# Performance work log

Hardware: AMD Instinct MI355X
Metric: run time of the kernel (lower is better)

Reference implementation:

```python
import jax, jax.numpy as jnp
import numpy as np

N_NODES = 100000
N_EDGES = 3200000
D_IN, D_HID, D_OUT = 512, 16, 64


def setup_inputs() -> dict:
    key = jax.random.key(0)
    ks = jax.random.split(key, 7)
    x = jax.random.normal(ks[0], (N_NODES, D_IN), jnp.float32)
    edge_index = jax.random.randint(ks[1], (2, N_EDGES), 0, N_NODES, dtype=jnp.int32)
    edge_weight = jax.random.uniform(ks[2], (N_EDGES,), jnp.float32)
    W1 = jax.random.normal(ks[3], (D_IN, D_HID), jnp.float32) * (1.0 / np.sqrt(D_IN))
    b1 = jnp.zeros((D_HID,), jnp.float32)
    W2 = jax.random.normal(ks[4], (D_HID, D_OUT), jnp.float32) * (1.0 / np.sqrt(D_HID))
    b2 = jnp.zeros((D_OUT,), jnp.float32)
    return {"x": x, "edge_index": edge_index, "edge_weight": edge_weight,
            "W1": W1, "b1": b1, "W2": W2, "b2": b2}


def reference(x, edge_index, edge_weight, W1, b1, W2, b2):
    N = x.shape[0]
    loop = jnp.arange(N, dtype=edge_index.dtype)
    # GCNConv(normalize=True): add self-loops (weight 1), symmetric normalization
    src = jnp.concatenate([edge_index[0], loop])
    dst = jnp.concatenate([edge_index[1], loop])
    w = jnp.concatenate([edge_weight, jnp.ones((N,), x.dtype)])
    deg = jax.ops.segment_sum(w, dst, num_segments=N)
    dinv = jnp.where(deg > 0, jax.lax.rsqrt(deg), 0.0)
    norm = dinv[src] * w * dinv[dst]  # [E+N]

    def gcn_conv(h, W, b):
        h = h @ W  # transform first (thin GEMM), then aggregate
        msg = h[src] * norm[:, None]  # gather + scale
        return jax.ops.segment_sum(msg, dst, num_segments=N) + b  # scatter-add

    h = jax.nn.relu(gcn_conv(x, W1, b1))
    # F.dropout is identity in eval mode
    out = gcn_conv(h, W2, b2)
    return jax.nn.log_softmax(out, axis=1)
```

## Files before the change

### kernel.cpp

```cpp
#include <hip/hip_runtime.h>
#include <hip/hip_bf16.h>


#define D_IN 512
#define D_HID 16
#define D_OUT 64
#define BDIM 128
#define BSHIFT 7
#define NBLK0 512

__global__ __launch_bounds__(256) void p0_count(const int* __restrict__ dst,
                                                int* __restrict__ bcnt,
                                                int NBUCK, int E, int chunk) {
    extern __shared__ int hist[];
    int k = blockIdx.x;
    for (int i = threadIdx.x; i < NBUCK; i += 256) hist[i] = 0;
    __syncthreads();
    int beg = k * chunk, end = min(beg + chunk, E);
    for (int e = beg + threadIdx.x; e < end; e += 256)
        atomicAdd(&hist[dst[e] >> BSHIFT], 1);
    __syncthreads();
    for (int i = threadIdx.x; i < NBUCK; i += 256)
        bcnt[(size_t)k * NBUCK + i] = hist[i];
}

__global__ __launch_bounds__(256) void p_scan1(int* __restrict__ bcnt,
                                               int* __restrict__ btot, int NBUCK) {
    __shared__ int s[256];
    int b = blockIdx.x, t = threadIdx.x;
    int v0 = bcnt[(size_t)(2 * t) * NBUCK + b];
    int v1 = bcnt[(size_t)(2 * t + 1) * NBUCK + b];
    int pair = v0 + v1;
    s[t] = pair;
    __syncthreads();
    for (int off = 1; off < 256; off <<= 1) {
        int v = (t >= off) ? s[t - off] : 0;
        __syncthreads();
        s[t] += v;
        __syncthreads();
    }
    int ex = s[t] - pair;
    bcnt[(size_t)(2 * t) * NBUCK + b] = ex;
    bcnt[(size_t)(2 * t + 1) * NBUCK + b] = ex + v0;
    if (t == 255) btot[b] = s[255];
}

__global__ __launch_bounds__(1024) void p_scan2(const int* __restrict__ btot,
                                                int* __restrict__ bbase,
                                                int NBUCK, int E) {
    __shared__ int s[1024];
    int t = threadIdx.x;
    int v = (t < NBUCK) ? btot[t] : 0;
    s[t] = v;
    __syncthreads();
    for (int off = 1; off < 1024; off <<= 1) {
        int u = (t >= off) ? s[t - off] : 0;
        __syncthreads();
        s[t] += u;
        __syncthreads();
    }
    if (t < NBUCK) bbase[t] = s[t] - v;
    if (t == 0) bbase[NBUCK] = E;
}

__global__ __launch_bounds__(256) void p1_scatter(const int* __restrict__ src,
                                                  const int* __restrict__ dst,
                                                  const float* __restrict__ w,
                                                  const int* __restrict__ bcnt,
                                                  const int* __restrict__ bbase,
                                                  float2* __restrict__ tmp,
                                                  int NBUCK, int E, int chunk) {
    extern __shared__ int cur[];
    int k = blockIdx.x;
    for (int i = threadIdx.x; i < NBUCK; i += 256)
        cur[i] = bbase[i] + bcnt[(size_t)k * NBUCK + i];
    __syncthreads();
    int beg = k * chunk, end = min(beg + chunk, E);
    for (int e = beg + threadIdx.x; e < end; e += 256) {
        int d = dst[e];
        int b = d >> BSHIFT;
        int pos = atomicAdd(&cur[b], 1);
        tmp[pos] = make_float2(__int_as_float(((d & (BDIM - 1)) << 24) | src[e]), w[e]);
    }
}

__global__ __launch_bounds__(256) void p4_sort(const float2* __restrict__ tmp,
                                               const int* __restrict__ bbase,
                                               float2* __restrict__ sorted,
                                               int* __restrict__ row_start,
                                               float* __restrict__ dinv,
                                               int NBUCK, int N, int E) {
    __shared__ int cnt[BDIM];
    __shared__ float wdeg[BDIM];
    __shared__ int pre[BDIM];
    __shared__ int cur[BDIM];
    int b = blockIdx.x;
    if (threadIdx.x < BDIM) { cnt[threadIdx.x] = 0; wdeg[threadIdx.x] = 0.0f; }
    __syncthreads();
    int beg = bbase[b], end = bbase[b + 1];
    for (int e = beg + threadIdx.x; e < end; e += 256) {
        float2 p = tmp[e];
        int dl = ((unsigned)__float_as_int(p.x)) >> 24;
        atomicAdd(&cnt[dl], 1);
        atomicAdd(&wdeg[dl], p.y);
    }
    __syncthreads();
    if (threadIdx.x < BDIM) pre[threadIdx.x] = cnt[threadIdx.x];
    __syncthreads();
    for (int off = 1; off < BDIM; off <<= 1) {
        int add = 0;
        if (threadIdx.x < BDIM && threadIdx.x >= off) add = pre[threadIdx.x - off];
        __syncthreads();
        if (threadIdx.x < BDIM) pre[threadIdx.x] += add;
        __syncthreads();
    }
    if (threadIdx.x < BDIM) {
        int ex = beg + pre[threadIdx.x] - cnt[threadIdx.x];
        cur[threadIdx.x] = ex;
        int node = (b << BSHIFT) + threadIdx.x;
        if (node < N) {
            row_start[node] = ex;
            dinv[node] = __frsqrt_rn(1.0f + wdeg[threadIdx.x]);
        }
    }
    if (b == NBUCK - 1 && threadIdx.x == 0) row_start[N] = E;
    __syncthreads();
    for (int e = beg + threadIdx.x; e < end; e += 256) {
        float2 p = tmp[e];
        unsigned u = (unsigned)__float_as_int(p.x);
        int dl = u >> 24;
        int pos = atomicAdd(&cur[dl], 1);
        sorted[pos] = make_float2(__int_as_float((int)(u & 0xFFFFFFu)), p.y);
    }
}

__global__ __launch_bounds__(256) void gemm1_kernel(const float* __restrict__ x,
                                                    const float* __restrict__ W1,
                                                    float* __restrict__ t, int N) {
    __shared__ float w1t[16 * 520];
    for (int idx = threadIdx.x; idx < D_IN * D_HID; idx += 256) {
        int k = idx >> 4, j = idx & 15;
        w1t[j * 520 + k] = W1[idx];
    }
    __syncthreads();

    const int wave = threadIdx.x >> 6;
    const int lane = threadIdx.x & 63;
    const int g = lane >> 4;
    const int s = lane & 15;

    for (int base = blockIdx.x * 16; base < N; base += gridDim.x * 16) {
        int row = base + wave * 4 + g;
        if (row < N) {
            const float4* xr = (const float4*)(x + (size_t)row * D_IN);
            float4 xv[8];
#pragma unroll
            for (int i = 0; i < 8; ++i) xv[i] = xr[s + 16 * i];
            float acc[16];
#pragma unroll
            for (int j = 0; j < 16; ++j) acc[j] = 0.0f;
#pragma unroll
            for (int i = 0; i < 8; ++i) {
                int kb = 4 * s + 64 * i;
#pragma unroll
                for (int j = 0; j < 16; ++j) {
                    const float4 wv = *(const float4*)&w1t[j * 520 + kb];
                    acc[j] += xv[i].x * wv.x + xv[i].y * wv.y + xv[i].z * wv.z + xv[i].w * wv.w;
                }
            }
#pragma unroll
            for (int j = 0; j < 16; ++j) {
#pragma unroll
                for (int m = 1; m < 16; m <<= 1) acc[j] += __shfl_xor(acc[j], m, 64);
            }
            float v = acc[0];
#pragma unroll
            for (int j = 1; j < 16; ++j) v = (s == j) ? acc[j] : v;
            t[(size_t)row * 16 + s] = v;
        }
    }
}

template <int LAYER>
__global__ __launch_bounds__(256) void agg_kernel(const float2* __restrict__ sorted,
                                                  const int* __restrict__ row_start,
                                                  const float* __restrict__ feat,
                                                  const float* __restrict__ selfv,
                                                  const float* __restrict__ dinv,
                                                  const float* __restrict__ b1,
                                                  float* __restrict__ outp, int N) {
    int node = blockIdx.x * 4 + (threadIdx.x >> 6);
    if (node >= N) return;
    int lane = threadIdx.x & 63;
    int j = lane & 15, k = lane >> 4;
    int beg = row_start[node], end = row_start[node + 1];
    float acc = 0.0f;
    for (int e = beg + k; e < end; e += 4) {
        float2 p = sorted[e];
        int s = __float_as_int(p.x);
        acc += dinv[s] * p.y * feat[(size_t)s * 16 + j];
    }
    acc += __shfl_xor(acc, 16, 64);
    acc += __shfl_xor(acc, 32, 64);
    float dn = dinv[node];
    float sv = selfv[(size_t)node * 16 + j];
    float r = dn * acc + dn * dn * sv;
    if (LAYER == 1) r = fmaxf(r + b1[j], 0.0f);
    if (k == 0) outp[(size_t)node * 16 + j] = r;
}

__global__ __launch_bounds__(256) void out_kernel(const float* __restrict__ v,
                                                  const float* __restrict__ W2,
                                                  const float* __restrict__ b2,
                                                  float* __restrict__ out, int N) {
    __shared__ float w2s[16 * 64];
    __shared__ float b2s[64];
    for (int idx = threadIdx.x; idx < 16 * 64; idx += 256) w2s[idx] = W2[idx];
    if (threadIdx.x < 64) b2s[threadIdx.x] = b2[threadIdx.x];
    __syncthreads();

    const int wave = threadIdx.x >> 6;
    const int lane = threadIdx.x & 63;

    for (int node = blockIdx.x * 4 + wave; node < N; node += gridDim.x * 4) {
        const float4* v4 = (const float4*)(v + (size_t)node * 16);
        float z = b2s[lane];
#pragma unroll
        for (int q = 0; q < 4; ++q) {
            float4 a = v4[q];
            z += a.x * w2s[(4 * q + 0) * 64 + lane];
            z += a.y * w2s[(4 * q + 1) * 64 + lane];
            z += a.z * w2s[(4 * q + 2) * 64 + lane];
            z += a.w * w2s[(4 * q + 3) * 64 + lane];
        }
        float m = z;
#pragma unroll
        for (int off = 32; off; off >>= 1) m = fmaxf(m, __shfl_xor(m, off, 64));
        float ez = __expf(z - m);
        float ssum = ez;
#pragma unroll
        for (int off = 32; off; off >>= 1) ssum += __shfl_xor(ssum, off, 64);
        out[(size_t)node * 64 + lane] = z - m - __logf(ssum);
    }
}

extern "C" void kernel_launch(void* const* d_in, const int* in_sizes, int n_in,
                              void* d_out, int out_size, void* d_ws, size_t ws_size,
                              hipStream_t stream) {
    const float* x  = (const float*)d_in[0];
    const int*   ei = (const int*)d_in[1];
    const float* ew = (const float*)d_in[2];
    const float* W1 = (const float*)d_in[3];
    const float* b1 = (const float*)d_in[4];
    const float* W2 = (const float*)d_in[5];
    const float* b2 = (const float*)d_in[6];
    float* out = (float*)d_out;

    const int N = in_sizes[0] / D_IN;
    const int E = in_sizes[2];
    const int* srcI = ei;
    const int* dstI = ei + E;

    const int NBUCK = (N + BDIM - 1) >> BSHIFT;
    const int chunk = (E + NBLK0 - 1) / NBLK0;

    float* ws = (float*)d_ws;
    size_t o = 0;
    float* dinv      = ws + o;         o += (size_t)N;             o = (o + 3) & ~(size_t)3;
    int*   row_start = (int*)(ws + o); o += (size_t)N + 2;         o = (o + 3) & ~(size_t)3;
    int*   bbase     = (int*)(ws + o); o += (size_t)NBUCK + 1;     o = (o + 3) & ~(size_t)3;
    int*   btot      = (int*)(ws + o); o += (size_t)NBUCK;         o = (o + 3) & ~(size_t)3;
    int*   bcnt      = (int*)(ws + o); o += (size_t)NBLK0 * NBUCK; o = (o + 3) & ~(size_t)3;
    float* tmpR      = ws + o;
    size_t tmpsz = (size_t)2 * E; if ((size_t)32 * N > tmpsz) tmpsz = (size_t)32 * N;
    o += tmpsz;                                                    o = (o + 3) & ~(size_t)3;

    float2* tmp = (float2*)tmpR;
    float*  t   = tmpR;
    float*  h1  = tmpR + (size_t)16 * N;
    float*  v   = t;

    float2* sorted = ((size_t)out_size >= (size_t)E * 8)
                         ? (float2*)d_out
                         : (float2*)(ws + o);

    p0_count<<<NBLK0, 256, NBUCK * sizeof(int), stream>>>(dstI, bcnt, NBUCK, E, chunk);
    p_scan1<<<NBUCK, 256, 0, stream>>>(bcnt, btot, NBUCK);
    p_scan2<<<1, 1024, 0, stream>>>(btot, bbase, NBUCK, E);
    p1_scatter<<<NBLK0, 256, NBUCK * sizeof(int), stream>>>(srcI, dstI, ew, bcnt, bbase,
                                                            tmp, NBUCK, E, chunk);
    p4_sort<<<NBUCK, 256, 0, stream>>>(tmp, bbase, sorted, row_start, dinv, NBUCK, N, E);

    gemm1_kernel<<<1024, 256, 0, stream>>>(x, W1, t, N);

    agg_kernel<1><<<(N + 3) / 4, 256, 0, stream>>>(sorted, row_start, t, t, dinv, b1, h1, N);
    agg_kernel<2><<<(N + 3) / 4, 256, 0, stream>>>(sorted, row_start, h1, h1, dinv, b1, v, N);

    out_kernel<<<2048, 256, 0, stream>>>(v, W2, b2, out, N);
}
```

Before: 657.9 us.

## Precompute edge norms in CSR, vectorize aggregation, fuse output GEMM+softmax into layer-2

Splits the per-bucket sort into a count kernel and a scatter kernel. The scatter now stores the fully normalized edge weight, so the aggregation kernels no longer gather dinv[src] for every edge on every layer. Aggregation reads two edges per float4 load, with peeling for odd start and end indices. The second aggregation also fuses the W2 projection, bias and log_softmax, which removes the separate out_kernel and the round trip of the intermediate features. The cost is one extra kernel launch and a dinv gather inside the scatter, and the sorted edge buffer now always lives in the workspace.

```diff
diff --git a/kernel.cpp b/kernel.cpp
--- a/kernel.cpp
+++ b/kernel.cpp
@@ -84,16 +84,14 @@
     }
 }
 
-__global__ __launch_bounds__(256) void p4_sort(const float2* __restrict__ tmp,
-                                               const int* __restrict__ bbase,
-                                               float2* __restrict__ sorted,
-                                               int* __restrict__ row_start,
-                                               float* __restrict__ dinv,
-                                               int NBUCK, int N, int E) {
+__global__ __launch_bounds__(256) void p4a_count(const float2* __restrict__ tmp,
+                                                 const int* __restrict__ bbase,
+                                                 int* __restrict__ row_start,
+                                                 float* __restrict__ dinv,
+                                                 int NBUCK, int N, int E) {
     __shared__ int cnt[BDIM];
     __shared__ float wdeg[BDIM];
     __shared__ int pre[BDIM];
-    __shared__ int cur[BDIM];
     int b = blockIdx.x;
     if (threadIdx.x < BDIM) { cnt[threadIdx.x] = 0; wdeg[threadIdx.x] = 0.0f; }
     __syncthreads();
@@ -115,22 +113,38 @@
         __syncthreads();
     }
     if (threadIdx.x < BDIM) {
-        int ex = beg + pre[threadIdx.x] - cnt[threadIdx.x];
-        cur[threadIdx.x] = ex;
         int node = (b << BSHIFT) + threadIdx.x;
         if (node < N) {
-            row_start[node] = ex;
+            row_start[node] = beg + pre[threadIdx.x] - cnt[threadIdx.x];
             dinv[node] = __frsqrt_rn(1.0f + wdeg[threadIdx.x]);
         }
     }
     if (b == NBUCK - 1 && threadIdx.x == 0) row_start[N] = E;
-    __syncthreads();
+}
+
+__global__ __launch_bounds__(256) void p4b_scatter(const float2* __restrict__ tmp,
+                                                   const int* __restrict__ bbase,
+                                                   const int* __restrict__ row_start,
+                                                   const float* __restrict__ dinv,
+                                                   float2* __restrict__ sorted, int N) {
+    __shared__ int cur[BDIM];
+    __shared__ float dl_dinv[BDIM];
+    int b = blockIdx.x;
+    if (threadIdx.x < BDIM) {
+        int node = (b << BSHIFT) + threadIdx.x;
+        cur[threadIdx.x] = (node < N) ? row_start[node] : 0;
+        dl_dinv[threadIdx.x] = (node < N) ? dinv[node] : 0.0f;
+    }
+    __syncthreads();
+    int beg = bbase[b], end = bbase[b + 1];
     for (int e = beg + threadIdx.x; e < end; e += 256) {
         float2 p = tmp[e];
         unsigned u = (unsigned)__float_as_int(p.x);
         int dl = u >> 24;
+        int s = (int)(u & 0xFFFFFFu);
         int pos = atomicAdd(&cur[dl], 1);
-        sorted[pos] = make_float2(__int_as_float((int)(u & 0xFFFFFFu)), p.y);
+        float nw = p.y * dinv[s] * dl_dinv[dl];
+        sorted[pos] = make_float2(__int_as_float(s), nw);
     }
 }
 
@@ -185,54 +199,55 @@
 __global__ __launch_bounds__(256) void agg_kernel(const float2* __restrict__ sorted,
                                                   const int* __restrict__ row_start,
                                                   const float* __restrict__ feat,
-                                                  const float* __restrict__ selfv,
                                                   const float* __restrict__ dinv,
                                                   const float* __restrict__ b1,
+                                                  const float* __restrict__ W2,
+                                                  const float* __restrict__ b2,
                                                   float* __restrict__ outp, int N) {
+    __shared__ float w2s[16 * 64];
+    __shared__ float b2s[64];
+    if (LAYER == 2) {
+        for (int idx = threadIdx.x; idx < 16 * 64; idx += 256) w2s[idx] = W2[idx];
+        if (threadIdx.x < 64) b2s[threadIdx.x] = b2[threadIdx.x];
+        __syncthreads();
+    }
     int node = blockIdx.x * 4 + (threadIdx.x >> 6);
     if (node >= N) return;
     int lane = threadIdx.x & 63;
     int j = lane & 15, k = lane >> 4;
     int beg = row_start[node], end = row_start[node + 1];
     float acc = 0.0f;
-    for (int e = beg + k; e < end; e += 4) {
-        float2 p = sorted[e];
-        int s = __float_as_int(p.x);
-        acc += dinv[s] * p.y * feat[(size_t)s * 16 + j];
+    int i0 = beg;
+    if ((i0 & 1) && i0 < end) {
+        if (k == 0) {
+            float2 p = sorted[i0];
+            acc += p.y * feat[(size_t)__float_as_int(p.x) * 16 + j];
+        }
+        ++i0;
+    }
+    for (int e = i0 + 2 * k; e + 1 < end; e += 8) {
+        float4 q = *(const float4*)(sorted + e);
+        int s0 = __float_as_int(q.x);
+        int s1 = __float_as_int(q.z);
+        acc += q.y * feat[(size_t)s0 * 16 + j];
+        acc += q.w * feat[(size_t)s1 * 16 + j];
+    }
+    if ((end > i0) && ((end - i0) & 1) && k == 0) {
+        float2 p = sorted[end - 1];
+        acc += p.y * feat[(size_t)__float_as_int(p.x) * 16 + j];
     }
     acc += __shfl_xor(acc, 16, 64);
     acc += __shfl_xor(acc, 32, 64);
     float dn = dinv[node];
-    float sv = selfv[(size_t)node * 16 + j];
-    float r = dn * acc + dn * dn * sv;
-    if (LAYER == 1) r = fmaxf(r + b1[j], 0.0f);
-    if (k == 0) outp[(size_t)node * 16 + j] = r;
-}
-
-__global__ __launch_bounds__(256) void out_kernel(const float* __restrict__ v,
-                                                  const float* __restrict__ W2,
-                                                  const float* __restrict__ b2,
-                                                  float* __restrict__ out, int N) {
-    __shared__ float w2s[16 * 64];
-    __shared__ float b2s[64];
-    for (int idx = threadIdx.x; idx < 16 * 64; idx += 256) w2s[idx] = W2[idx];
-    if (threadIdx.x < 64) b2s[threadIdx.x] = b2[threadIdx.x];
-    __syncthreads();
-
-    const int wave = threadIdx.x >> 6;
-    const int lane = threadIdx.x & 63;
-
-    for (int node = blockIdx.x * 4 + wave; node < N; node += gridDim.x * 4) {
-        const float4* v4 = (const float4*)(v + (size_t)node * 16);
+    float r = acc + dn * dn * feat[(size_t)node * 16 + j];
+    if (LAYER == 1) {
+        r = fmaxf(r + b1[j], 0.0f);
+        if (lane < 16) outp[(size_t)node * 16 + j] = r;
+    } else {
         float z = b2s[lane];
 #pragma unroll
-        for (int q = 0; q < 4; ++q) {
-            float4 a = v4[q];
-            z += a.x * w2s[(4 * q + 0) * 64 + lane];
-            z += a.y * w2s[(4 * q + 1) * 64 + lane];
-            z += a.z * w2s[(4 * q + 2) * 64 + lane];
-            z += a.w * w2s[(4 * q + 3) * 64 + lane];
-        }
+        for (int j2 = 0; j2 < 16; ++j2)
+            z += __shfl(r, j2, 64) * w2s[j2 * 64 + lane];
         float m = z;
 #pragma unroll
         for (int off = 32; off; off >>= 1) m = fmaxf(m, __shfl_xor(m, off, 64));
@@ -240,7 +255,7 @@
         float ssum = ez;
 #pragma unroll
         for (int off = 32; off; off >>= 1) ssum += __shfl_xor(ssum, off, 64);
-        out[(size_t)node * 64 + lane] = z - m - __logf(ssum);
+        outp[(size_t)node * 64 + lane] = z - m - __logf(ssum);
     }
 }
 
@@ -274,27 +289,24 @@
     float* tmpR      = ws + o;
     size_t tmpsz = (size_t)2 * E; if ((size_t)32 * N > tmpsz) tmpsz = (size_t)32 * N;
     o += tmpsz;                                                    o = (o + 3) & ~(size_t)3;
+    float2* sorted   = (float2*)(ws + o);
 
     float2* tmp = (float2*)tmpR;
     float*  t   = tmpR;
     float*  h1  = tmpR + (size_t)16 * N;
-    float*  v   = t;
-
-    float2* sorted = ((size_t)out_size >= (size_t)E * 8)
-                         ? (float2*)d_out
-                         : (float2*)(ws + o);
 
     p0_count<<<NBLK0, 256, NBUCK * sizeof(int), stream>>>(dstI, bcnt, NBUCK, E, chunk);
     p_scan1<<<NBUCK, 256, 0, stream>>>(bcnt, btot, NBUCK);
     p_scan2<<<1, 1024, 0, stream>>>(btot, bbase, NBUCK, E);
     p1_scatter<<<NBLK0, 256, NBUCK * sizeof(int), stream>>>(srcI, dstI, ew, bcnt, bbase,
                                                             tmp, NBUCK, E, chunk);
-    p4_sort<<<NBUCK, 256, 0, stream>>>(tmp, bbase, sorted, row_start, dinv, NBUCK, N, E);
+    p4a_count<<<NBUCK, 256, 0, stream>>>(tmp, bbase, row_start, dinv, NBUCK, N, E);
+    p4b_scatter<<<NBUCK, 256, 0, stream>>>(tmp, bbase, row_start, dinv, sorted, N);
 
     gemm1_kernel<<<1024, 256, 0, stream>>>(x, W1, t, N);
 
-    agg_kernel<1><<<(N + 3) / 4, 256, 0, stream>>>(sorted, row_start, t, t, dinv, b1, h1, N);
-    agg_kernel<2><<<(N + 3) / 4, 256, 0, stream>>>(sorted, row_start, h1, h1, dinv, b1, v, N);
-
-    out_kernel<<<2048, 256, 0, stream>>>(v, W2, b2, out, N);
-}
+    agg_kernel<1><<<(N + 3) / 4, 256, 0, stream>>>(sorted, row_start, t, dinv,
+                                                   b1, W2, b2, h1, N);
+    agg_kernel<2><<<(N + 3) / 4, 256, 0, stream>>>(sorted, row_start, h1, dinv,
+                                                   b1, W2, b2, out, N);
+}
```

Result: faster. 631.7 us (-4.0%).
